# Kernel optimization log

Hardware: AMD Instinct MI355X
Metric: run time of the kernel (lower is better)

## Reference

```python
import jax, jax.numpy as jnp
import numpy as np

TAU = 1.0
ATOL = 1e-06
MAX_ITER = 64  # bisection halves the bracket each iter; 64 iters reaches fp32 precision
N_WORKERS = 64
D = 2097152  # 2**21 coordinates


def setup_inputs() -> dict:
    key = jax.random.key(0)
    y = jax.random.normal(key, (N_WORKERS, D), dtype=jnp.float32)
    return {"y": y}


def reference(y) -> jnp.ndarray:
    # Coordinate-wise smooth (erf-based) median via bisection.
    # torch code transposes y and reduces over the last dim; equivalently we
    # reduce over the worker axis (axis 0) and keep per-coordinate state [d].
    xl = jnp.min(y, axis=0)  # [d] lower bracket
    xg = jnp.max(y, axis=0)  # [d] upper bracket

    def body(_, carry):
        xl, xg = carry
        xm = 0.5 * (xl + xg)                                  # [d]
        fm = jnp.sum(jax.lax.erf((y - xm) / TAU), axis=0)     # [d]
        left = fm > 0
        xl = jnp.where(left, xm, xl)
        xg = jnp.where(left, xg, xm)
        return xl, xg

    # Fixed trip count (no host-sync early exit). After MAX_ITER=64 halvings the
    # bracket width is far below the torch atol=1e-6 break threshold, so the
    # result matches the torch early-exit version to well within atol.
    xl, xg = jax.lax.fori_loop(0, MAX_ITER, body, (xl, xg))
    return 0.5 * (xl + xg)  # [d]
```

## Files before the change

kernel.cpp:

```cpp
#include <hip/hip_runtime.h>

typedef float v2f __attribute__((ext_vector_type(2)));

#define NW 64
#define NP 32
#define MAX_EVALS 12
#define FREEZE_TOL 2e-3f

__global__ __launch_bounds__(256, 4) void damed_median_kernel(
    const float* __restrict__ y, float* __restrict__ out, int D) {
  int d = blockIdx.x * blockDim.x + threadIdx.x;
  if (d >= D) return;

  v2f v[NP];
  v2f vmin = {3.4e38f, 3.4e38f}, vmax = {-3.4e38f, -3.4e38f}, sum2 = {0.f, 0.f};
#pragma unroll
  for (int p = 0; p < NP; ++p) {
    v2f t;
    t.x = y[(size_t)(2 * p) * (size_t)D + (size_t)d];
    t.y = y[(size_t)(2 * p + 1) * (size_t)D + (size_t)d];
    v[p] = t;
    vmin = __builtin_elementwise_min(vmin, t);
    vmax = __builtin_elementwise_max(vmax, t);
    sum2 += t;
  }
  float xl = fminf(vmin.x, vmin.y);
  float xg = fmaxf(vmax.x, vmax.y);
  float x = (sum2.x + sum2.y) * (1.0f / NW);
  x = fminf(fmaxf(x, xl), xg);

  const float B1 = 0.278393f, B2 = 0.230389f, B3 = 0.000972f, B4 = 0.078108f;
  const v2f one2 = {1.f, 1.f};
  const v2f Q1 = {B1, B1}, Q2 = {B2, B2}, Q3 = {B3, B3}, Q4 = {B4, B4};
  const v2f P1 = {B1, B1}, P2 = {2 * B2, 2 * B2};
  const v2f P3 = {3 * B3, 3 * B3}, P4 = {4 * B4, 4 * B4};

  bool frozen = false;
#pragma unroll 1
  for (int e = 0; e < MAX_EVALS; ++e) {
    v2f fmA = {0.f, 0.f}, fmB = {0.f, 0.f}, fdA = {0.f, 0.f}, fdB = {0.f, 0.f};
    v2f nx = {-x, -x};
#pragma unroll
    for (int p = 0; p < NP; p += 2) {
      v2f tA = v[p] + nx;
      v2f tB = v[p + 1] + nx;
      v2f aA, aB;
      aA.x = __builtin_fabsf(tA.x); aA.y = __builtin_fabsf(tA.y);
      aB.x = __builtin_fabsf(tB.x); aB.y = __builtin_fabsf(tB.y);
      v2f qA = __builtin_elementwise_fma(aA, Q4, Q3);
      v2f qB = __builtin_elementwise_fma(aB, Q4, Q3);
      qA = __builtin_elementwise_fma(aA, qA, Q2);
      qB = __builtin_elementwise_fma(aB, qB, Q2);
      qA = __builtin_elementwise_fma(aA, qA, Q1);
      qB = __builtin_elementwise_fma(aB, qB, Q1);
      qA = __builtin_elementwise_fma(aA, qA, one2);
      qB = __builtin_elementwise_fma(aB, qB, one2);
      v2f dA = __builtin_elementwise_fma(aA, P4, P3);
      v2f dB = __builtin_elementwise_fma(aB, P4, P3);
      dA = __builtin_elementwise_fma(aA, dA, P2);
      dB = __builtin_elementwise_fma(aB, dB, P2);
      dA = __builtin_elementwise_fma(aA, dA, P1);
      dB = __builtin_elementwise_fma(aB, dB, P1);
      v2f rA, rB;
      rA.x = __builtin_amdgcn_rcpf(qA.x); rA.y = __builtin_amdgcn_rcpf(qA.y);
      rB.x = __builtin_amdgcn_rcpf(qB.x); rB.y = __builtin_amdgcn_rcpf(qB.y);
      v2f r2A = rA * rA, r2B = rB * rB;
      v2f r4A = r2A * r2A, r4B = r2B * r2B;
      v2f r5A = r4A * rA, r5B = r4B * rB;
      fdA = __builtin_elementwise_fma(r5A, dA, fdA);
      fdB = __builtin_elementwise_fma(r5B, dB, fdB);
      v2f eA = one2 - r4A;
      v2f eB = one2 - r4B;
      eA.x = __builtin_copysignf(eA.x, tA.x); eA.y = __builtin_copysignf(eA.y, tA.y);
      eB.x = __builtin_copysignf(eB.x, tB.x); eB.y = __builtin_copysignf(eB.y, tB.y);
      fmA += eA; fmB += eB;
    }
    v2f fm2 = fmA + fmB, fd2 = fdA + fdB;
    float fm = fm2.x + fm2.y;
    float fd = 4.0f * (fd2.x + fd2.y);

    if (fm > 0.f) xl = x; else xg = x;
    float xn = x + fm * __builtin_amdgcn_rcpf(fd);
    bool ok = (xn >= xl) && (xn <= xg);
    float cand = ok ? xn : 0.5f * (xl + xg);
    float st = __builtin_fabsf(cand - x);
    float xnew = frozen ? x : cand;
    frozen = frozen || (st <= FREEZE_TOL);
    x = xnew;
    if (__all(frozen)) break;
  }
  out[d] = x;
}

extern "C" void kernel_launch(void* const* d_in, const int* in_sizes, int n_in,
                              void* d_out, int out_size, void* d_ws, size_t ws_size,
                              hipStream_t stream) {
  const float* y = (const float*)d_in[0];
  float* out = (float*)d_out;
  const int D = out_size;
  const int threads = 256;
  const int blocks = (D + threads - 1) / threads;
  damed_median_kernel<<<blocks, threads, 0, stream>>>(y, out, D);
}
```

Before: 140.4 us.

## Replace Newton iterations with secant steps after first Newton evaluation

After one Newton step that evaluates both the erf sum and its derivative, later iterations use a secant update that needs only the function value. This drops the derivative polynomial, the r^5 products and the derivative accumulators from each later evaluation, leaving less ALU work per iteration. The freeze tolerance is also loosened and the maximum number of evaluations cut, so loops exit sooner at some cost in accuracy. Secant steps converge more slowly than Newton steps and could need more iterations, and the looser tolerance may push results closer to the error limit.

```diff
diff --git a/kernel.cpp b/kernel.cpp
--- a/kernel.cpp
+++ b/kernel.cpp
@@ -4,8 +4,8 @@
 
 #define NW 64
 #define NP 32
-#define MAX_EVALS 12
-#define FREEZE_TOL 2e-3f
+#define MAX_EVALS 10
+#define FREEZE_TOL 4.5e-3f
 
 __global__ __launch_bounds__(256, 4) void damed_median_kernel(
     const float* __restrict__ y, float* __restrict__ out, int D) {
@@ -35,9 +35,41 @@
   const v2f P1 = {B1, B1}, P2 = {2 * B2, 2 * B2};
   const v2f P3 = {3 * B3, 3 * B3}, P4 = {4 * B4, 4 * B4};
 
-  bool frozen = false;
-#pragma unroll 1
-  for (int e = 0; e < MAX_EVALS; ++e) {
+  auto evalF = [&](float xc) -> float {
+    v2f fmA = {0.f, 0.f}, fmB = {0.f, 0.f};
+    v2f nx = {-xc, -xc};
+#pragma unroll
+    for (int p = 0; p < NP; p += 2) {
+      v2f tA = v[p] + nx;
+      v2f tB = v[p + 1] + nx;
+      v2f aA, aB;
+      aA.x = __builtin_fabsf(tA.x); aA.y = __builtin_fabsf(tA.y);
+      aB.x = __builtin_fabsf(tB.x); aB.y = __builtin_fabsf(tB.y);
+      v2f qA = __builtin_elementwise_fma(aA, Q4, Q3);
+      v2f qB = __builtin_elementwise_fma(aB, Q4, Q3);
+      qA = __builtin_elementwise_fma(aA, qA, Q2);
+      qB = __builtin_elementwise_fma(aB, qB, Q2);
+      qA = __builtin_elementwise_fma(aA, qA, Q1);
+      qB = __builtin_elementwise_fma(aB, qB, Q1);
+      qA = __builtin_elementwise_fma(aA, qA, one2);
+      qB = __builtin_elementwise_fma(aB, qB, one2);
+      v2f rA, rB;
+      rA.x = __builtin_amdgcn_rcpf(qA.x); rA.y = __builtin_amdgcn_rcpf(qA.y);
+      rB.x = __builtin_amdgcn_rcpf(qB.x); rB.y = __builtin_amdgcn_rcpf(qB.y);
+      rA = rA * rA; rB = rB * rB;
+      rA = rA * rA; rB = rB * rB;
+      v2f eA = one2 - rA;
+      v2f eB = one2 - rB;
+      eA.x = __builtin_copysignf(eA.x, tA.x); eA.y = __builtin_copysignf(eA.y, tA.y);
+      eB.x = __builtin_copysignf(eB.x, tB.x); eB.y = __builtin_copysignf(eB.y, tB.y);
+      fmA += eA; fmB += eB;
+    }
+    v2f s = fmA + fmB;
+    return s.x + s.y;
+  };
+
+  float fm0, fd0;
+  {
     v2f fmA = {0.f, 0.f}, fmB = {0.f, 0.f}, fdA = {0.f, 0.f}, fdB = {0.f, 0.f};
     v2f nx = {-x, -x};
 #pragma unroll
@@ -76,18 +108,31 @@
       fmA += eA; fmB += eB;
     }
     v2f fm2 = fmA + fmB, fd2 = fdA + fdB;
-    float fm = fm2.x + fm2.y;
-    float fd = 4.0f * (fd2.x + fd2.y);
+    fm0 = fm2.x + fm2.y;
+    fd0 = 4.0f * (fd2.x + fd2.y);
+  }
+  if (fm0 > 0.f) xl = x; else xg = x;
+  float xn = x + fm0 * __builtin_amdgcn_rcpf(fd0);
+  bool ok = (xn >= xl) && (xn <= xg);
+  float cand = ok ? xn : 0.5f * (xl + xg);
+  bool frozen = (__builtin_fabsf(cand - x) <= FREEZE_TOL);
+  float xprev = x, fmprev = fm0;
+  x = cand;
 
-    if (fm > 0.f) xl = x; else xg = x;
-    float xn = x + fm * __builtin_amdgcn_rcpf(fd);
-    bool ok = (xn >= xl) && (xn <= xg);
-    float cand = ok ? xn : 0.5f * (xl + xg);
-    float st = __builtin_fabsf(cand - x);
-    float xnew = frozen ? x : cand;
+#pragma unroll 1
+  for (int e = 1; e < MAX_EVALS; ++e) {
+    if (__all(frozen)) break;
+    float fmc = evalF(x);
+    if (fmc > 0.f) xl = x; else xg = x;
+    float xs = x + fmc * (x - xprev) / (fmprev - fmc);
+    bool ok2 = (xs >= xl) && (xs <= xg);
+    float cand2 = ok2 ? xs : 0.5f * (xl + xg);
+    float st = __builtin_fabsf(cand2 - x);
+    float xnew = frozen ? x : cand2;
+    xprev = frozen ? xprev : x;
+    fmprev = frozen ? fmprev : fmc;
     frozen = frozen || (st <= FREEZE_TOL);
     x = xnew;
-    if (__all(frozen)) break;
   }
   out[d] = x;
 }
```

Measured after the change: 118.9 us. 1.18x faster.
